# Optimization experiments

Measured on AMD Instinct MI355X. Metric: run time of the kernel, lower is better.

## Reference

```python
import jax, jax.numpy as jnp
import numpy as np

NUM_HEADS = 8
IN_CH = 256  # C per branch; x has 2*C channels
DHW = (16, 16, 16)


def _proj(w, b, feat):
    # 1x1x1 Conv3d == per-voxel linear over channels. w: [Co, Ci], feat: [B, Ci, D, H, W]
    return jnp.einsum('oc,bcdhw->bodhw', w, feat) + b[None, :, None, None, None]


def _rope(n, dim):
    # matches rotary_embedding: returns [dim, n]
    inv_freq = 1.0 / (10000.0 ** (jnp.arange(0, dim, 2, dtype=jnp.float32) / dim))
    pos = jnp.linspace(-1.0, 1.0, n)
    sinusoid = pos[:, None] * inv_freq[None, :]          # [n, dim//2]
    emb = jnp.concatenate([jnp.sin(sinusoid), jnp.cos(sinusoid)], axis=-1)  # [n, dim]
    return emb.T                                          # [dim, n]


def setup_inputs() -> dict:
    key = jax.random.key(0)
    ks = jax.random.split(key, 5)
    D, H, W = DHW
    C = IN_CH
    s = 0.05
    return {
        'x': jax.random.normal(ks[0], (1, 2 * C, D, H, W), dtype=jnp.float32),
        'wq': jax.random.normal(ks[1], (C, C), dtype=jnp.float32) * s,
        'bq': jnp.zeros((C,), jnp.float32),
        'wk': jax.random.normal(ks[2], (C, C), dtype=jnp.float32) * s,
        'bk': jnp.zeros((C,), jnp.float32),
        'wv': jax.random.normal(ks[3], (C, C), dtype=jnp.float32) * s,
        'bv': jnp.zeros((C,), jnp.float32),
        'wo': jax.random.normal(ks[4], (2 * C, C), dtype=jnp.float32) * s,
        'bo': jnp.zeros((2 * C,), jnp.float32),
    }


def reference(x, wq, bq, wk, bk, wv, bv, wo, bo):
    qf, kvf = jnp.split(x, 2, axis=1)          # each [B, C, D, H, W]
    B, C, D, H, W = qf.shape
    hd = C // NUM_HEADS
    N = D * H * W
    q = _proj(wq, bq, qf).reshape(B, NUM_HEADS, hd, N)
    k = _proj(wk, bk, kvf).reshape(B, NUM_HEADS, hd, N)
    v = _proj(wv, bv, kvf).reshape(B, NUM_HEADS, hd, N)
    pe = _rope(N, hd)                           # [hd, N]
    q = q * pe[None, None]
    k = k * pe[None, None]
    attn = jnp.einsum('bhcn,bhcm->bhnm', q, k)  # note: no 1/sqrt(d) scaling, as in source
    attn = jax.nn.softmax(attn, axis=-1)
    out = jnp.einsum('bhnm,bhcm->bhcn', attn, v).reshape(B, C, D, H, W)
    return _proj(wo, bo, out + qf)              # [B, 2C, D, H, W]
```

## Files before the change

kernel.cpp:

```cpp
#include <hip/hip_runtime.h>
#include <hip/hip_bf16.h>

#define CIN 256
#define NV 4096
#define NHEAD 8
#define HD 32
#define NSPLIT 4
#define KSPAN (NV / NSPLIT)
#define LOG2E 1.44269504088896340736f
#define LOG2_10K_16 0.8304820237218405f

typedef __attribute__((ext_vector_type(8))) short short8;
typedef __attribute__((ext_vector_type(4))) float f32x4;

static __device__ __forceinline__ unsigned short f2bf(float f) {
    union { float f; unsigned u; } v; v.f = f;
    unsigned r = v.u + 0x7fffu + ((v.u >> 16) & 1u);
    return (unsigned short)(r >> 16);
}
static __device__ __forceinline__ unsigned pk_bf2(float x0, float x1) {
    return __builtin_amdgcn_perm(__float_as_uint(x1), __float_as_uint(x0),
                                 0x07060302u);
}
static __device__ __forceinline__ float bflo(unsigned u) {
    return __uint_as_float(u << 16);
}
static __device__ __forceinline__ float bfhi(unsigned u) {
    return __uint_as_float(u & 0xffff0000u);
}

__global__ __launch_bounds__(256) void conv_w(
    const float* __restrict__ wq, const float* __restrict__ wk,
    const float* __restrict__ wv, const float* __restrict__ wo,
    unsigned short* __restrict__ Wb)
{
    int i = (blockIdx.x * 256 + threadIdx.x) * 4;
    if (i >= 327680) return;
    const float* src;
    int off = i;
    if (i < 65536) { src = wq; }
    else if (i < 131072) { src = wk; off = i - 65536; }
    else if (i < 196608) { src = wv; off = i - 131072; }
    else { src = wo; off = i - 196608; }
    float4 v = *(const float4*)&src[off];
    unsigned short pk[4] = {f2bf(v.x), f2bf(v.y), f2bf(v.z), f2bf(v.w)};
    *(uint2*)&Wb[i] = *(uint2*)pk;
}

__global__ __launch_bounds__(512) void qkv_fused(
    const float* __restrict__ x, const unsigned short* __restrict__ Wb,
    const float* __restrict__ bq, const float* __restrict__ bk,
    const float* __restrict__ bv,
    unsigned short* __restrict__ Qbf, unsigned short* __restrict__ Kbf,
    unsigned short* __restrict__ Vbf)
{
    const int which = blockIdx.z;
    const unsigned short* Wp = Wb + (size_t)which * 65536;
    const float* Bp = (which == 0) ? bq : (which == 1) ? bk : bv;
    const int cbase = (which == 0) ? 0 : CIN;

    const int n0 = blockIdx.x * 32;
    const int m0 = blockIdx.y * 128;
    const int t = threadIdx.x;

    __shared__ __align__(16) unsigned short Sbuf[32 * 264];

    {
        const int n = t & 31, cg = t >> 5;
#pragma unroll 4
        for (int cc = 0; cc < 16; cc += 2) {
            const int c = cg * 16 + cc;
            size_t off = (size_t)(cbase + c) * NV + n0 + n;
            *(unsigned*)&Sbuf[n * 264 + c] = pk_bf2(x[off], x[off + NV]);
        }
    }
    __syncthreads();

    const int w = t >> 6;
    const int lane = t & 63;
    const int ln = lane & 15;
    const int quad = lane >> 4;
    const int M = m0 + w * 16 + ln;

    f32x4 acc[2] = {};
    const unsigned short* Wrow = &Wp[(size_t)M * 256 + quad * 8];
    for (int k0 = 0; k0 < 256; k0 += 32) {
        short8 a = *(const short8*)&Wrow[k0];
        short8 b[2];
#pragma unroll
        for (int nt = 0; nt < 2; ++nt)
            b[nt] = *(const short8*)&Sbuf[(nt * 16 + ln) * 264 + k0 + quad * 8];
        if (which == 2) {
#pragma unroll
            for (int nt = 0; nt < 2; ++nt)
                acc[nt] = __builtin_amdgcn_mfma_f32_16x16x32_bf16(
                    b[nt], a, acc[nt], 0, 0, 0);
        } else {
#pragma unroll
            for (int nt = 0; nt < 2; ++nt)
                acc[nt] = __builtin_amdgcn_mfma_f32_16x16x32_bf16(
                    a, b[nt], acc[nt], 0, 0, 0);
        }
    }
    __syncthreads();

    if (which == 2) {
        const int cl = w * 16 + ln;
        const float bias = Bp[m0 + cl];
#pragma unroll
        for (int nt = 0; nt < 2; ++nt) {
            unsigned short pk4[4];
#pragma unroll
            for (int r = 0; r < 4; ++r) pk4[r] = f2bf(acc[nt][r] + bias);
            *(uint2*)&Sbuf[cl * 40 + nt * 16 + quad * 4] = *(uint2*)pk4;
        }
        __syncthreads();
        {
            const int cl2 = t >> 2, q = t & 3;
            uint2 lo = *(const uint2*)&Sbuf[cl2 * 40 + q * 4];
            uint2 hi = *(const uint2*)&Sbuf[cl2 * 40 + 16 + q * 4];
            uint4 v;
            v.x = lo.x; v.y = lo.y; v.z = hi.x; v.w = hi.y;
            *(uint4*)&Vbf[(size_t)(m0 + cl2) * NV + n0 + q * 8] = v;
        }
    } else {
        const int mb = m0 + w * 16 + quad * 4;
        const int cb = mb & 31;
        const float qscale = (which == 0) ? LOG2E : 1.0f;
        float bias[4], invf[4];
#pragma unroll
        for (int r = 0; r < 4; ++r) {
            bias[r] = Bp[mb + r];
            invf[r] = __builtin_amdgcn_exp2f(
                -(float)((cb + r) & 15) * LOG2_10K_16);
        }
        const bool use_sin = (cb < 16);
        const int ml = w * 16 + quad * 4;
#pragma unroll
        for (int nt = 0; nt < 2; ++nt) {
            const int n = n0 + nt * 16 + ln;
            const float pos = (float)n * (2.0f / 4095.0f) - 1.0f;
#pragma unroll
            for (int r = 0; r < 4; ++r) {
                float ang = pos * invf[r];
                float f = (use_sin ? __sinf(ang) : __cosf(ang)) * qscale;
                Sbuf[(nt * 16 + ln) * 264 + ml + r] =
                    f2bf((acc[nt][r] + bias[r]) * f);
            }
        }
        __syncthreads();
        unsigned short* dst = (which == 0) ? Qbf : Kbf;
        const int h0 = m0 >> 5;
        {
            const int hh = t >> 7;
            const int n = (t >> 2) & 31;
            const int cw = t & 3;
            uint4 v = *(const uint4*)&Sbuf[n * 264 + hh * 32 + cw * 8];
            *(uint4*)&dst[((size_t)(h0 + hh) * NV + n0 + n) * HD + cw * 8] = v;
        }
    }
}

__global__ __launch_bounds__(256, 4) void attn_mfma(
    const unsigned short* __restrict__ Qbf,
    const unsigned short* __restrict__ Kbf,
    const unsigned short* __restrict__ Vbf,
    unsigned short* __restrict__ Opartb, float* __restrict__ Lpart)
{
    const int h = blockIdx.y;
    const int q0 = blockIdx.x * 64;
    const int z = blockIdx.z;
    const int kbase = z * KSPAN;
    const int t = threadIdx.x;
    const int w = t >> 6;
    const int lane = t & 63;
    const int ln = lane & 15;
    const int quad = lane >> 4;

    __shared__ __align__(16) unsigned short Ks[2][2048];
    __shared__ __align__(16) unsigned short Vs[2][2048];

    const short8 qa = *(const short8*)
        &Qbf[((size_t)h * NV + q0 + w * 16 + ln) * HD + quad * 8];

    const unsigned short* Kh = Kbf + (size_t)h * NV * HD;
    const unsigned short* Vh = Vbf + (size_t)h * HD * NV;

    const int cv = t >> 3;
    const unsigned short* gsrcV = Vh + (size_t)cv * NV + ((t & 7) ^ (cv & 7)) * 8;
    const int kv = t >> 2;
    const unsigned short* gsrcK =
        Kh + (size_t)kv * HD + ((t & 3) ^ (kv & 3)) * 8;

    f32x4 oacc[2] = {};
    f32x4 lacc = {};
    const short vone = (short)0x3F80;
    const short8 vones = {vone, vone, vone, vone, vone, vone, vone, vone};

    __builtin_amdgcn_global_load_lds(
        (const __attribute__((address_space(1))) unsigned int*)(gsrcK +
            (size_t)kbase * HD),
        (__attribute__((address_space(3))) unsigned int*)&Ks[0][t * 8], 16, 0, 0);
    __builtin_amdgcn_global_load_lds(
        (const __attribute__((address_space(1))) unsigned int*)(gsrcV + kbase),
        (__attribute__((address_space(3))) unsigned int*)&Vs[0][t * 8], 16, 0, 0);
    __syncthreads();

    const int sgk = (quad ^ (ln & 3)) * 8;
    for (int i = 0; i < KSPAN / 64; ++i) {
        const int kb = kbase + i * 64;
        const int buf = i & 1;

        if (i + 1 < KSPAN / 64) {
            __builtin_amdgcn_global_load_lds(
                (const __attribute__((address_space(1))) unsigned int*)(gsrcK +
                    (size_t)(kb + 64) * HD),
                (__attribute__((address_space(3))) unsigned int*)&Ks[buf ^ 1][t * 8],
                16, 0, 0);
            __builtin_amdgcn_global_load_lds(
                (const __attribute__((address_space(1))) unsigned int*)(gsrcV +
                    kb + 64),
                (__attribute__((address_space(3))) unsigned int*)&Vs[buf ^ 1][t * 8],
                16, 0, 0);
        }

        f32x4 s[4];
#pragma unroll
        for (int ct = 0; ct < 4; ++ct) {
            const short8 kf = *(const short8*)
                &Ks[buf][(ct * 16 + ln) * 32 + sgk];
            f32x4 z4 = {0.f, 0.f, 0.f, 0.f};
            s[ct] = __builtin_amdgcn_mfma_f32_16x16x32_bf16(kf, qa, z4,
                                                            0, 0, 0);
        }

        float p[4][4];
#pragma unroll
        for (int ct = 0; ct < 4; ++ct)
#pragma unroll
            for (int r = 0; r < 4; ++r)
                p[ct][r] = __builtin_amdgcn_exp2f(s[ct][r]);

#pragma unroll
        for (int h2 = 0; h2 < 2; ++h2) {
            short8 pa;
            unsigned* pau = (unsigned*)&pa;
            pau[0] = pk_bf2(p[2 * h2][0], p[2 * h2][1]);
            pau[1] = pk_bf2(p[2 * h2][2], p[2 * h2][3]);
            pau[2] = pk_bf2(p[2 * h2 + 1][0], p[2 * h2 + 1][1]);
            pau[3] = pk_bf2(p[2 * h2 + 1][2], p[2 * h2 + 1][3]);
            lacc = __builtin_amdgcn_mfma_f32_16x16x32_bf16(pa, vones, lacc,
                                                           0, 0, 0);
#pragma unroll
            for (int ctile = 0; ctile < 2; ++ctile) {
                const int cA = ctile * 16 + ln;
                const short8 vb = *(const short8*)
                    &Vs[buf][cA * 64 + (((h2 * 4 + quad) ^ (cA & 7)) * 8)];
                oacc[ctile] = __builtin_amdgcn_mfma_f32_16x16x32_bf16(
                    pa, vb, oacc[ctile], 0, 0, 0);
            }
        }
        __syncthreads();
    }

    unsigned short* Oz = Opartb + (size_t)z * CIN * NV;
    float* Lz = Lpart + (size_t)z * NHEAD * NV;
    if (ln == 0) {
#pragma unroll
        for (int r = 0; r < 4; ++r)
            Lz[(size_t)h * NV + q0 + w * 16 + quad * 4 + r] = lacc[r];
    }
#pragma unroll
    for (int ctile = 0; ctile < 2; ++ctile) {
        uint2 st;
        st.x = pk_bf2(oacc[ctile][0], oacc[ctile][1]);
        st.y = pk_bf2(oacc[ctile][2], oacc[ctile][3]);
        *(uint2*)&Oz[(size_t)(h * HD + ctile * 16 + ln) * NV + q0 + w * 16 +
                     quad * 4] = st;
    }
}

__global__ __launch_bounds__(512) void out_fused(
    const float* __restrict__ x,
    const unsigned short* __restrict__ Opartb,
    const float* __restrict__ Lpart,
    const unsigned short* __restrict__ Wob, const float* __restrict__ bo,
    float* __restrict__ out)
{
    const int n0 = blockIdx.x * 32;
    const int m0 = blockIdx.y * 128;
    const int t = threadIdx.x;

    __shared__ __align__(16) unsigned short Ys[32 * 264];

    {
        const int n2 = (t & 15) * 2;
        const int grp = t >> 4;
        const int h = grp >> 2;
        const size_t lo = (size_t)h * NV + n0 + n2;
        float l0 = 0.f, l1 = 0.f;
#pragma unroll
        for (int zz = 0; zz < NSPLIT; ++zz) {
            l0 += Lpart[(size_t)zz * NHEAD * NV + lo];
            l1 += Lpart[(size_t)zz * NHEAD * NV + lo + 1];
        }
        const float rl0 = __builtin_amdgcn_rcpf(l0);
        const float rl1 = __builtin_amdgcn_rcpf(l1);
#pragma unroll
        for (int i = 0; i < 8; ++i) {
            const int c = grp * 8 + i;
            size_t off = (size_t)c * NV + n0 + n2;
            float s0 = 0.f, s1 = 0.f;
#pragma unroll
            for (int zz = 0; zz < NSPLIT; ++zz) {
                unsigned o = *(const unsigned*)&Opartb[(size_t)zz * CIN * NV + off];
                s0 += bflo(o);
                s1 += bfhi(o);
            }
            float2 x2 = *(const float2*)&x[off];
            Ys[n2 * 264 + c] = f2bf(s0 * rl0 + x2.x);
            Ys[(n2 + 1) * 264 + c] = f2bf(s1 * rl1 + x2.y);
        }
    }
    __syncthreads();

    const int w = t >> 6;
    const int lane = t & 63;
    const int ln = lane & 15;
    const int quad = lane >> 4;
    const int M = m0 + w * 16 + ln;

    const unsigned short* Wrow = &Wob[(size_t)M * 256 + quad * 8];
    f32x4 acc[2] = {};
    for (int k0 = 0; k0 < 256; k0 += 32) {
        short8 a = *(const short8*)&Wrow[k0];
        short8 b[2];
#pragma unroll
        for (int nt = 0; nt < 2; ++nt)
            b[nt] = *(const short8*)&Ys[(nt * 16 + ln) * 264 + k0 + quad * 8];
#pragma unroll
        for (int nt = 0; nt < 2; ++nt)
            acc[nt] = __builtin_amdgcn_mfma_f32_16x16x32_bf16(
                a, b[nt], acc[nt], 0, 0, 0);
    }

    const int mb = m0 + w * 16 + quad * 4;
    float bias[4];
#pragma unroll
    for (int r = 0; r < 4; ++r) bias[r] = bo[mb + r];
#pragma unroll
    for (int nt = 0; nt < 2; ++nt)
#pragma unroll
        for (int r = 0; r < 4; ++r)
            out[(size_t)(mb + r) * NV + n0 + nt * 16 + ln] =
                acc[nt][r] + bias[r];
}

extern "C" void kernel_launch(void* const* d_in, const int* in_sizes, int n_in,
                              void* d_out, int out_size, void* d_ws,
                              size_t ws_size, hipStream_t stream)
{
    const float* x  = (const float*)d_in[0];
    const float* wq = (const float*)d_in[1];
    const float* bq = (const float*)d_in[2];
    const float* wk = (const float*)d_in[3];
    const float* bk = (const float*)d_in[4];
    const float* wv = (const float*)d_in[5];
    const float* bv = (const float*)d_in[6];
    const float* wo = (const float*)d_in[7];
    const float* bo = (const float*)d_in[8];
    float* out = (float*)d_out;

    unsigned short* Wb  = (unsigned short*)d_ws;
    unsigned short* Qbf = Wb + 327680;
    unsigned short* Kbf = Qbf + (size_t)CIN * NV;
    unsigned short* Vbf = Kbf + (size_t)CIN * NV;
    float* Lpart = (float*)(Vbf + (size_t)CIN * NV);
    unsigned short* Opartb =
        (unsigned short*)(Lpart + NSPLIT * (size_t)NHEAD * NV);

    conv_w<<<dim3(320), 256, 0, stream>>>(wq, wk, wv, wo, Wb);
    qkv_fused<<<dim3(128, 2, 3), 512, 0, stream>>>(
        x, Wb, bq, bk, bv, Qbf, Kbf, Vbf);
    attn_mfma<<<dim3(NV / 64, NHEAD, NSPLIT), 256, 0, stream>>>(
        Qbf, Kbf, Vbf, Opartb, Lpart);
    out_fused<<<dim3(128, 4), 512, 0, stream>>>(
        x, Opartb, Lpart, Wb + 196608, bo, out);
}
```

Measured before the change: 119.8 us.

## Double K/V stage to 128 keys, remap block order, add MFMA priority hints

The attention kernel now loads 128 keys per pipeline stage instead of 64, which halves the number of barriers and loop iterations. It also remaps the linear block index so that consecutive blocks share a query tile across heads and splits, and wraps the MFMA sections in s_setprio. These target barrier overhead and L2 locality, and help the MFMAs issue ahead of the exp work. The cost is double the LDS use (32KB per block), which may cut occupancy under the 4-blocks-per-SM launch bound.

```diff
diff --git a/kernel.cpp b/kernel.cpp
--- a/kernel.cpp
+++ b/kernel.cpp
@@ -167,9 +167,11 @@
     const unsigned short* __restrict__ Vbf,
     unsigned short* __restrict__ Opartb, float* __restrict__ Lpart)
 {
-    const int h = blockIdx.y;
-    const int q0 = blockIdx.x * 64;
-    const int z = blockIdx.z;
+    const int l = blockIdx.x + (blockIdx.y << 6) + (blockIdx.z << 9);
+    const int pr = l & 31;
+    const int h = pr & 7;
+    const int z = pr >> 3;
+    const int q0 = (l >> 5) * 64;
     const int kbase = z * KSPAN;
     const int t = threadIdx.x;
     const int w = t >> 6;
@@ -177,8 +179,8 @@
     const int ln = lane & 15;
     const int quad = lane >> 4;
 
-    __shared__ __align__(16) unsigned short Ks[2][2048];
-    __shared__ __align__(16) unsigned short Vs[2][2048];
+    __shared__ __align__(16) unsigned short Ks[2 * 4096];
+    __shared__ __align__(16) unsigned short Vs[2 * 4096];
 
     const short8 qa = *(const short8*)
         &Qbf[((size_t)h * NV + q0 + w * 16 + ln) * HD + quad * 8];
@@ -200,64 +202,96 @@
     __builtin_amdgcn_global_load_lds(
         (const __attribute__((address_space(1))) unsigned int*)(gsrcK +
             (size_t)kbase * HD),
-        (__attribute__((address_space(3))) unsigned int*)&Ks[0][t * 8], 16, 0, 0);
+        (__attribute__((address_space(3))) unsigned int*)&Ks[t * 8], 16, 0, 0);
+    __builtin_amdgcn_global_load_lds(
+        (const __attribute__((address_space(1))) unsigned int*)(gsrcK +
+            (size_t)(kbase + 64) * HD),
+        (__attribute__((address_space(3))) unsigned int*)&Ks[2048 + t * 8],
+        16, 0, 0);
     __builtin_amdgcn_global_load_lds(
         (const __attribute__((address_space(1))) unsigned int*)(gsrcV + kbase),
-        (__attribute__((address_space(3))) unsigned int*)&Vs[0][t * 8], 16, 0, 0);
+        (__attribute__((address_space(3))) unsigned int*)&Vs[t * 8], 16, 0, 0);
+    __builtin_amdgcn_global_load_lds(
+        (const __attribute__((address_space(1))) unsigned int*)(gsrcV + kbase +
+            64),
+        (__attribute__((address_space(3))) unsigned int*)&Vs[2048 + t * 8],
+        16, 0, 0);
     __syncthreads();
 
     const int sgk = (quad ^ (ln & 3)) * 8;
-    for (int i = 0; i < KSPAN / 64; ++i) {
-        const int kb = kbase + i * 64;
-        const int buf = i & 1;
-
-        if (i + 1 < KSPAN / 64) {
+    for (int i = 0; i < KSPAN / 128; ++i) {
+        const int kb = kbase + i * 128;
+        const int buf = (i & 1) * 4096;
+
+        if (i + 1 < KSPAN / 128) {
+            const int nb = buf ^ 4096;
             __builtin_amdgcn_global_load_lds(
                 (const __attribute__((address_space(1))) unsigned int*)(gsrcK +
-                    (size_t)(kb + 64) * HD),
-                (__attribute__((address_space(3))) unsigned int*)&Ks[buf ^ 1][t * 8],
+                    (size_t)(kb + 128) * HD),
+                (__attribute__((address_space(3))) unsigned int*)&Ks[nb + t * 8],
+                16, 0, 0);
+            __builtin_amdgcn_global_load_lds(
+                (const __attribute__((address_space(1))) unsigned int*)(gsrcK +
+                    (size_t)(kb + 192) * HD),
+                (__attribute__((address_space(3))) unsigned int*)&Ks[nb + 2048 +
+                    t * 8],
                 16, 0, 0);
             __builtin_amdgcn_global_load_lds(
                 (const __attribute__((address_space(1))) unsigned int*)(gsrcV +
-                    kb + 64),
-                (__attribute__((address_space(3))) unsigned int*)&Vs[buf ^ 1][t * 8],
+                    kb + 128),
+                (__attribute__((address_space(3))) unsigned int*)&Vs[nb + t * 8],
                 16, 0, 0);
-        }
-
-        f32x4 s[4];
-#pragma unroll
-        for (int ct = 0; ct < 4; ++ct) {
-            const short8 kf = *(const short8*)
-                &Ks[buf][(ct * 16 + ln) * 32 + sgk];
-            f32x4 z4 = {0.f, 0.f, 0.f, 0.f};
-            s[ct] = __builtin_amdgcn_mfma_f32_16x16x32_bf16(kf, qa, z4,
-                                                            0, 0, 0);
-        }
-
-        float p[4][4];
-#pragma unroll
-        for (int ct = 0; ct < 4; ++ct)
-#pragma unroll
-            for (int r = 0; r < 4; ++r)
-                p[ct][r] = __builtin_amdgcn_exp2f(s[ct][r]);
-
-#pragma unroll
-        for (int h2 = 0; h2 < 2; ++h2) {
-            short8 pa;
-            unsigned* pau = (unsigned*)&pa;
-            pau[0] = pk_bf2(p[2 * h2][0], p[2 * h2][1]);
-            pau[1] = pk_bf2(p[2 * h2][2], p[2 * h2][3]);
-            pau[2] = pk_bf2(p[2 * h2 + 1][0], p[2 * h2 + 1][1]);
-            pau[3] = pk_bf2(p[2 * h2 + 1][2], p[2 * h2 + 1][3]);
-            lacc = __builtin_amdgcn_mfma_f32_16x16x32_bf16(pa, vones, lacc,
-                                                           0, 0, 0);
-#pragma unroll
-            for (int ctile = 0; ctile < 2; ++ctile) {
-                const int cA = ctile * 16 + ln;
-                const short8 vb = *(const short8*)
-                    &Vs[buf][cA * 64 + (((h2 * 4 + quad) ^ (cA & 7)) * 8)];
-                oacc[ctile] = __builtin_amdgcn_mfma_f32_16x16x32_bf16(
-                    pa, vb, oacc[ctile], 0, 0, 0);
+            __builtin_amdgcn_global_load_lds(
+                (const __attribute__((address_space(1))) unsigned int*)(gsrcV +
+                    kb + 192),
+                (__attribute__((address_space(3))) unsigned int*)&Vs[nb + 2048 +
+                    t * 8],
+                16, 0, 0);
+        }
+
+#pragma unroll
+        for (int hf = 0; hf < 2; ++hf) {
+            const int sb = buf + hf * 2048;
+
+            f32x4 s[4];
+            __builtin_amdgcn_s_setprio(1);
+#pragma unroll
+            for (int ct = 0; ct < 4; ++ct) {
+                const short8 kf = *(const short8*)
+                    &Ks[sb + (ct * 16 + ln) * 32 + sgk];
+                f32x4 z4 = {0.f, 0.f, 0.f, 0.f};
+                s[ct] = __builtin_amdgcn_mfma_f32_16x16x32_bf16(kf, qa, z4,
+                                                                0, 0, 0);
+            }
+            __builtin_amdgcn_s_setprio(0);
+
+            float p[4][4];
+#pragma unroll
+            for (int ct = 0; ct < 4; ++ct)
+#pragma unroll
+                for (int r = 0; r < 4; ++r)
+                    p[ct][r] = __builtin_amdgcn_exp2f(s[ct][r]);
+
+#pragma unroll
+            for (int h2 = 0; h2 < 2; ++h2) {
+                short8 pa;
+                unsigned* pau = (unsigned*)&pa;
+                pau[0] = pk_bf2(p[2 * h2][0], p[2 * h2][1]);
+                pau[1] = pk_bf2(p[2 * h2][2], p[2 * h2][3]);
+                pau[2] = pk_bf2(p[2 * h2 + 1][0], p[2 * h2 + 1][1]);
+                pau[3] = pk_bf2(p[2 * h2 + 1][2], p[2 * h2 + 1][3]);
+                __builtin_amdgcn_s_setprio(1);
+                lacc = __builtin_amdgcn_mfma_f32_16x16x32_bf16(pa, vones, lacc,
+                                                               0, 0, 0);
+#pragma unroll
+                for (int ctile = 0; ctile < 2; ++ctile) {
+                    const int cA = ctile * 16 + ln;
+                    const short8 vb = *(const short8*)
+                        &Vs[sb + cA * 64 + (((h2 * 4 + quad) ^ (cA & 7)) * 8)];
+                    oacc[ctile] = __builtin_amdgcn_mfma_f32_16x16x32_bf16(
+                        pa, vb, oacc[ctile], 0, 0, 0);
+                }
+                __builtin_amdgcn_s_setprio(0);
             }
         }
         __syncthreads();
```

Result: slower. 122.2 us (+2.1%).
